# Optimization experiments

Hardware: AMD Instinct MI355X
Metric: run time of the kernel (lower is better)

Reference implementation:

```python
import jax, jax.numpy as jnp
import numpy as np

N, E, G = 10000, 80000, 64
F_IN, D, EA, H = 14, 64, 4, 128


def setup_inputs() -> dict:
    key = jax.random.key(0)
    ks = jax.random.split(key, 16)
    f32 = jnp.float32
    def nrm(k, shape, s=0.1):
        return jax.random.normal(k, shape, f32) * s
    return {
        "x": jax.random.normal(ks[0], (N, F_IN), f32),
        "edge_index": jax.random.randint(ks[1], (2, E), 0, N),
        "edge_attr": jax.random.uniform(ks[2], (E, EA), f32),
        "batch": jnp.sort(jax.random.randint(ks[3], (N,), 0, G)),
        "do_dropout": 0,
        "lin0_w": nrm(ks[4], (F_IN, D)), "lin0_b": jnp.zeros((D,), f32),
        "h1_w": nrm(ks[5], (EA, H)), "h1_b": jnp.zeros((H,), f32),
        "h2_w": nrm(ks[6], (H, D * D), 0.02), "h2_b": jnp.zeros((D * D,), f32),
        "conv_root": nrm(ks[7], (D, D)), "conv_bias": jnp.zeros((D,), f32),
        "gru_w_ih": nrm(ks[8], (3 * D, D)), "gru_w_hh": nrm(ks[9], (3 * D, D)),
        "gru_b_ih": jnp.zeros((3 * D,), f32), "gru_b_hh": jnp.zeros((3 * D,), f32),
        "lstm_w_ih": nrm(ks[10], (4 * D, 2 * D)), "lstm_w_hh": nrm(ks[11], (4 * D, D)),
        "lstm_b_ih": jnp.zeros((4 * D,), f32), "lstm_b_hh": jnp.zeros((4 * D,), f32),
        "lin1_w": nrm(ks[12], (2 * D, D)), "lin1_b": jnp.zeros((D,), f32),
        "lin2_w": nrm(ks[13], (D, 1)), "lin2_b": jnp.zeros((1,), f32),
    }


def _seg_softmax(e, seg, n):
    m = jax.ops.segment_max(e, seg, num_segments=n)
    ex = jnp.exp(e - m[seg])
    s = jax.ops.segment_sum(ex, seg, num_segments=n)
    return ex / s[seg]


def _forward(x, edge_index, edge_attr, batch,
             lin0_w, lin0_b, h1_w, h1_b, h2_w, h2_b, conv_root, conv_bias,
             gru_w_ih, gru_w_hh, gru_b_ih, gru_b_hh,
             lstm_w_ih, lstm_w_hh, lstm_b_ih, lstm_b_hh,
             lin1_w, lin1_b, lin2_w, lin2_b):
    src, tgt = edge_index[0], edge_index[1]
    out = jax.nn.relu(x @ lin0_w + lin0_b)              # [N, D]
    h = out
    # edge-conditioned weights: MLP(edge_attr) -> [E, D, D]
    W_e = (jax.nn.relu(edge_attr @ h1_w + h1_b) @ h2_w + h2_b).reshape(E, D, D)
    deg = jax.ops.segment_sum(jnp.ones((E,), out.dtype), tgt, num_segments=N)
    deg = jnp.maximum(deg, 1.0)[:, None]
    for _ in range(3):
        msg = jnp.einsum("ei,eio->eo", out[src], W_e)   # per-edge matmul
        agg = jax.ops.segment_sum(msg, tgt, num_segments=N) / deg  # mean aggr
        m = jax.nn.relu(agg + out @ conv_root + conv_bias)
        # single GRU step (torch nn.GRU, 1 layer, seq_len=1)
        gi = m @ gru_w_ih.T + gru_b_ih
        gh = h @ gru_w_hh.T + gru_b_hh
        ir, iz, in_ = jnp.split(gi, 3, axis=-1)
        hr, hz, hn = jnp.split(gh, 3, axis=-1)
        r = jax.nn.sigmoid(ir + hr)
        z = jax.nn.sigmoid(iz + hz)
        n = jnp.tanh(in_ + r * hn)
        h = (1.0 - z) * n + z * h
        out = h
    # Set2Set pooling, 3 processing steps
    q_star = jnp.zeros((G, 2 * D), out.dtype)
    hs = jnp.zeros((G, D), out.dtype)
    cs = jnp.zeros((G, D), out.dtype)
    for _ in range(3):
        gates = q_star @ lstm_w_ih.T + lstm_b_ih + hs @ lstm_w_hh.T + lstm_b_hh
        i, f, g, o = jnp.split(gates, 4, axis=-1)
        cs = jax.nn.sigmoid(f) * cs + jax.nn.sigmoid(i) * jnp.tanh(g)
        hs = jax.nn.sigmoid(o) * jnp.tanh(cs)
        q = hs                                          # [G, D]
        e = jnp.sum(out * q[batch], axis=-1)            # [N]
        a = _seg_softmax(e, batch, G)
        r = jax.ops.segment_sum(a[:, None] * out, batch, num_segments=G)
        q_star = jnp.concatenate([q, r], axis=-1)
    y = jax.nn.relu(q_star @ lin1_w + lin1_b)
    # do_dropout=False in this reference (eval mode): dropout is identity
    y = y @ lin2_w + lin2_b
    return y.reshape(-1)


def reference(x, edge_index, edge_attr, batch, do_dropout,
              lin0_w, lin0_b, h1_w, h1_b, h2_w, h2_b, conv_root, conv_bias,
              gru_w_ih, gru_w_hh, gru_b_ih, gru_b_hh,
              lstm_w_ih, lstm_w_hh, lstm_b_ih, lstm_b_hh,
              lin1_w, lin1_b, lin2_w, lin2_b):
    return _forward(x, edge_index, edge_attr, batch,
                    lin0_w, lin0_b, h1_w, h1_b, h2_w, h2_b, conv_root, conv_bias,
                    gru_w_ih, gru_w_hh, gru_b_ih, gru_b_hh,
                    lstm_w_ih, lstm_w_hh, lstm_b_ih, lstm_b_hh,
                    lin1_w, lin1_b, lin2_w, lin2_b)
```

## Files before the change

kernel.cpp:

```cpp
#include <hip/hip_runtime.h>
#include <math.h>

#define N_NODES 10000
#define N_EDGES 80000
#define N_GRAPH 64
#define DD 64
#define HIDW 128
#define F_IN 14
#define EAD 4
#define KSMAX 8

typedef _Float16 f16x8 __attribute__((ext_vector_type(8)));
typedef float f32x4 __attribute__((ext_vector_type(4)));

__device__ __forceinline__ float sigmoidf_(float x){ return 1.0f/(1.0f+expf(-x)); }


__global__ void k_prep_bpack(const float* __restrict__ h2w, _Float16* __restrict__ Bp){
  int idx = blockIdx.x*256 + threadIdx.x;
  if (idx >= (HIDW*DD/32)*4*64*8) return;
  int j = idx & 7, l = (idx >> 3) & 63, cg = (idx >> 9) & 3, st = idx >> 11;
  int k = st*32 + ((l >> 4) << 3) + j;
  int o = cg*16 + (l & 15);
  int h = k >> 6, i = k & 63;
  Bp[idx] = (_Float16)h2w[(size_t)h*4096 + i*64 + o];
}

__global__ void k_prep_wT(const float* __restrict__ gih, const float* __restrict__ ghh,
                          const float* __restrict__ lih, const float* __restrict__ lhh,
                          float* __restrict__ WihT, float* __restrict__ WhhT,
                          float* __restrict__ IhT,  float* __restrict__ HhT){
  int idx = blockIdx.x*256 + threadIdx.x;
  if (idx < 12288){ int k=idx/192, j=idx%192; WihT[idx]=gih[j*64+k]; return; }
  idx -= 12288;
  if (idx < 12288){ int k=idx/192, j=idx%192; WhhT[idx]=ghh[j*64+k]; return; }
  idx -= 12288;
  if (idx < 32768){ int k=idx>>8, j=idx&255; IhT[idx]=lih[j*128+k]; return; }
  idx -= 32768;
  if (idx < 16384){ int k=idx>>8, j=idx&255; HhT[idx]=lhh[j*64+k]; return; }
}


__global__ void k_count(const int* __restrict__ tgt, int* __restrict__ cnt){
  int e = blockIdx.x*256 + threadIdx.x;
  if (e < N_EDGES) atomicAdd(&cnt[tgt[e]], 1);
}

__global__ __launch_bounds__(1024) void k_scan(const int* __restrict__ cnt, int* __restrict__ offs,
                                               int* __restrict__ cursor, float* __restrict__ deg){
  __shared__ int sc[1024];
  int t = threadIdx.x;
  int base = t*10;
  int loc[10]; int tot = 0;
  #pragma unroll
  for (int j=0;j<10;++j){
    int i = base+j;
    int c = (i < N_NODES) ? cnt[i] : 0;
    loc[j] = tot; tot += c;
  }
  sc[t] = tot; __syncthreads();
  for (int st=1; st<1024; st<<=1){
    int v = (t>=st) ? sc[t-st] : 0;
    __syncthreads();
    sc[t] += v;
    __syncthreads();
  }
  int ex = sc[t] - tot;
  #pragma unroll
  for (int j=0;j<10;++j){
    int i = base+j;
    if (i < N_NODES){
      int o = ex + loc[j];
      offs[i] = o; cursor[i] = o;
      int c = cnt[i];
      deg[i] = (float)(c > 0 ? c : 1);
    }
  }
  if (t == 1023) offs[N_NODES] = sc[1023];
}

__global__ void k_sortE(const int* __restrict__ tgt, int* __restrict__ cursor, int* __restrict__ sorted){
  int e = blockIdx.x*256 + threadIdx.x;
  if (e < N_EDGES){ int p = atomicAdd(&cursor[tgt[e]], 1); sorted[p] = e; }
}

__global__ void k_graphoff(const int* __restrict__ batch, int* __restrict__ goff){
  int g = threadIdx.x;
  if (g > N_GRAPH) return;
  int lo = 0, hi = N_NODES;
  while (lo < hi){ int mid = (lo+hi)>>1; if (batch[mid] < g) lo = mid+1; else hi = mid; }
  goff[g] = lo;
}


__global__ __launch_bounds__(256) void k_lin0(const float* __restrict__ x, const float* __restrict__ w,
                                              const float* __restrict__ b, float* __restrict__ s){
  int tid = threadIdx.x;
  int g = tid >> 6, o = tid & 63;
  int n = blockIdx.x*4 + g;
  __shared__ float xL[4][F_IN];
  if (tid < 4*F_IN){
    int gg = tid / F_IN, k = tid % F_IN;
    int nn = blockIdx.x*4 + gg;
    xL[gg][k] = (nn < N_NODES) ? x[nn*F_IN + k] : 0.f;
  }
  __syncthreads();
  if (n >= N_NODES) return;
  float acc = b[o];
  #pragma unroll
  for (int k=0;k<F_IN;++k) acc += xL[g][k]*w[k*64+o];
  s[n*64+o] = fmaxf(acc, 0.f);
}


template<int CH, bool WRITE_S>
__global__ __launch_bounds__(256) void k_aggpre_t(
    const float* __restrict__ s, const float* __restrict__ ea,
    const float* __restrict__ h1_w, const float* __restrict__ h1_b,
    const int* __restrict__ offs, const int* __restrict__ sorted,
    const int* __restrict__ srcA, int c0,
    _Float16* __restrict__ P, float* __restrict__ Ssum){
  constexpr int RH = CH/4;
  int t = blockIdx.x;
  int tid = threadIdx.x;
  int i = tid & 63, hb = tid >> 6;
  __shared__ float sL[4][64];
  __shared__ float hidL[4][CH];
  __shared__ int eIdx[4], sIdx[4];
  float acc[RH];
  #pragma unroll
  for (int r=0;r<RH;++r) acc[r]=0.f;
  float sacc = 0.f;
  int e0 = offs[t], e1 = offs[t+1];
  for (int base = e0; base < e1; base += 4){
    int ecnt = min(4, e1 - base);
    __syncthreads();
    if (tid < ecnt){
      int e = sorted[base + tid];
      eIdx[tid] = e;
      sIdx[tid] = srcA[e];
    }
    __syncthreads();
    if (hb < ecnt) sL[hb][i] = s[(size_t)sIdx[hb]*64 + i];
    for (int a = tid; a < 4*CH; a += 256){
      int j = a / CH, hh = a % CH;
      if (j < ecnt){
        int e = eIdx[j];
        int h = c0 + hh;
        float v = h1_b[h];
        #pragma unroll
        for (int k=0;k<EAD;++k) v += ea[e*EAD+k]*h1_w[k*HIDW + h];
        hidL[j][hh] = fmaxf(v, 0.f);
      }
    }
    __syncthreads();
    for (int j=0;j<ecnt;++j){
      float sv = sL[j][i];
      #pragma unroll
      for (int r=0;r<RH;++r) acc[r] += hidL[j][hb*RH + r]*sv;
      if (WRITE_S && hb==0) sacc += sv;
    }
  }
  _Float16* row = P + (size_t)t*(CH*64);
  #pragma unroll
  for (int r=0;r<RH;++r) row[(hb*RH + r)*64 + i] = (_Float16)acc[r];
  if (WRITE_S && hb==0) Ssum[(size_t)t*64 + i] = sacc;
}

__global__ __launch_bounds__(256) void k_gemm_lds(const _Float16* __restrict__ A,
    const _Float16* __restrict__ Bp, float* __restrict__ Cpart, int K, int first){
  __shared__ _Float16 tile[16*1024];
  int tid = threadIdx.x;
  int y = blockIdx.y;
  const size_t rowBytes = (size_t)K*2;
  {
    int sub = tid >> 7;
    int colb = (tid & 127) * 16;
    const char* Abase = (const char*)A + (size_t)(blockIdx.x*16)*rowBytes + (size_t)y*2048;
    #pragma unroll
    for (int i = 0; i < 8; ++i){
      int r = i*2 + sub;
      f16x8 v = *(const f16x8*)(Abase + (size_t)r*rowBytes + (size_t)(colb ^ ((r&7)<<4)));
      *(f16x8*)((char*)tile + r*2048 + colb) = v;
    }
  }
  __syncthreads();
  int cg = tid >> 6, lane = tid & 63;
  int row = lane & 15, kb = lane >> 4;
  const char* tbase = (const char*)tile + row*2048;
  int swz = (row & 7) << 4;
  f32x4 acc = 0.f;
  int fr0 = y*32*4;
  #pragma unroll 8
  for (int st = 0; st < 32; ++st){
    f16x8 af = *(const f16x8*)(tbase + ((st*64 + kb*16) ^ swz));
    f16x8 bf = *(const f16x8*)(Bp + ((size_t)(fr0 + st*4 + cg)*64 + lane)*8);
    acc = __builtin_amdgcn_mfma_f32_16x16x32_f16(af, bf, acc, 0, 0, 0);
  }
  int crow0 = blockIdx.x*16 + kb*4;
  int ccol = cg*16 + (lane & 15);
  float* base = Cpart + (size_t)y*(N_NODES*64);
  #pragma unroll
  for (int r=0;r<4;++r){
    float* cp = base + (size_t)(crow0 + r)*64 + ccol;
    if (first) *cp = acc[r];
    else       *cp += acc[r];
  }
}

__global__ __launch_bounds__(256) void k_node_update(const float* __restrict__ Cpart,
    const float* __restrict__ Ssum, const float* __restrict__ h2b,
    const float* __restrict__ deg, float* __restrict__ s,
    const float* __restrict__ conv_root, const float* __restrict__ conv_bias,
    const float* __restrict__ WihT, const float* __restrict__ WhhT,
    const float* __restrict__ bih, const float* __restrict__ bhh, int nslots){
  int tid = threadIdx.x;
  int g = tid >> 6, o = tid & 63;
  int n = blockIdx.x*4 + g;
  __shared__ float hS[4][DD];
  __shared__ float mS[4][DD];
  __shared__ float ssS[4][DD];
  bool valid = n < N_NODES;
  float hold = valid ? s[(size_t)n*DD + o] : 0.f;
  hS[g][o] = hold;
  ssS[g][o] = valid ? Ssum[(size_t)n*DD + o] : 0.f;
  __syncthreads();
  float a = 0.f;
  if (valid){
    for (int ks=0; ks<nslots; ++ks) a += Cpart[(size_t)ks*(N_NODES*64) + (size_t)n*64 + o];
  }
  #pragma unroll 8
  for (int k=0;k<DD;++k) a += ssS[g][k]*h2b[k*64+o];
  float dinv = valid ? 1.0f/deg[n] : 0.f;
  float acc = a*dinv + conv_bias[o];
  #pragma unroll 8
  for (int k=0;k<DD;++k) acc += hS[g][k]*conv_root[k*64+o];
  float m = fmaxf(acc, 0.f);
  mS[g][o] = m;
  __syncthreads();
  float gi0 = bih[o], gi1 = bih[64+o], gi2 = bih[128+o];
  float gh0 = bhh[o], gh1 = bhh[64+o], gh2 = bhh[128+o];
  for (int k=0;k<DD;++k){
    float mk = mS[g][k], hk = hS[g][k];
    gi0 += mk*WihT[k*192 + o];      gh0 += hk*WhhT[k*192 + o];
    gi1 += mk*WihT[k*192 + 64 + o]; gh1 += hk*WhhT[k*192 + 64 + o];
    gi2 += mk*WihT[k*192 + 128+ o]; gh2 += hk*WhhT[k*192 + 128+ o];
  }
  float r = sigmoidf_(gi0+gh0);
  float z = sigmoidf_(gi1+gh1);
  float nn = tanhf(gi2 + r*gh2);
  float hnew = (1.f - z)*nn + z*hold;
  if (valid) s[(size_t)n*DD + o] = hnew;
}


__global__ __launch_bounds__(256) void k_set2set(const float* __restrict__ sND,
    const int* __restrict__ goff,
    const float* __restrict__ IhT, const float* __restrict__ HhT,
    const float* __restrict__ bih, const float* __restrict__ bhh,
    float* __restrict__ qstarOut){
  int g = blockIdx.x;
  int tid = threadIdx.x;
  int lane = tid & 63, w = tid >> 6;
  __shared__ float qL[2*DD];
  __shared__ float hL[DD];
  __shared__ float cL[DD];
  __shared__ float gate[256];
  __shared__ float red[4];
  __shared__ float red2[4][DD];
  if (tid < 2*DD) qL[tid] = 0.f;
  if (tid < DD){ hL[tid] = 0.f; cL[tid] = 0.f; }
  __syncthreads();
  int n0 = goff[g], n1 = goff[g+1];
  for (int st = 0; st < 3; ++st){
    float acc = bih[tid] + bhh[tid];
    #pragma unroll 8
    for (int k=0;k<2*DD;++k) acc += qL[k]*IhT[k*256 + tid];
    #pragma unroll 8
    for (int k=0;k<DD;++k)   acc += hL[k]*HhT[k*256 + tid];
    gate[tid] = acc;
    __syncthreads();
    if (tid < DD){
      float i = sigmoidf_(gate[tid]);
      float f = sigmoidf_(gate[64+tid]);
      float gg = tanhf(gate[128+tid]);
      float o = sigmoidf_(gate[192+tid]);
      float c = f*cL[tid] + i*gg;
      float h = o*tanhf(c);
      cL[tid] = c; hL[tid] = h;
    }
    __syncthreads();
    float wmax = -INFINITY;
    for (int n = n0 + w; n < n1; n += 4){
      float p = sND[(size_t)n*DD + lane] * hL[lane];
      #pragma unroll
      for (int s2=32; s2>0; s2>>=1) p += __shfl_xor(p, s2, 64);
      wmax = fmaxf(wmax, p);
    }
    if (lane == 0) red[w] = wmax;
    __syncthreads();
    float m = fmaxf(fmaxf(red[0], red[1]), fmaxf(red[2], red[3]));
    __syncthreads();
    float wsum = 0.f, racc = 0.f;
    for (int n = n0 + w; n < n1; n += 4){
      float outv = sND[(size_t)n*DD + lane];
      float p = outv * hL[lane];
      #pragma unroll
      for (int s2=32; s2>0; s2>>=1) p += __shfl_xor(p, s2, 64);
      float ex = expf(p - m);
      wsum += ex;
      racc += ex * outv;
    }
    if (lane == 0) red[w] = wsum;
    red2[w][lane] = racc;
    __syncthreads();
    if (tid < DD){
      float stot = red[0]+red[1]+red[2]+red[3];
      float rsum = red2[0][tid]+red2[1][tid]+red2[2][tid]+red2[3][tid];
      float r = (stot > 0.f) ? rsum/stot : 0.f;
      qL[tid] = hL[tid];
      qL[DD + tid] = r;
    }
    __syncthreads();
  }
  if (tid < 2*DD) qstarOut[g*2*DD + tid] = qL[tid];
}

__global__ __launch_bounds__(256) void k_final(const float* __restrict__ qstar,
    const float* __restrict__ lin1_w, const float* __restrict__ lin1_b,
    const float* __restrict__ lin2_w, const float* __restrict__ lin2_b,
    float* __restrict__ out){
  __shared__ float red[256];
  int tid = threadIdx.x;
  int g = tid >> 2, part = tid & 3;
  float acc = 0.f;
  for (int d = part*16; d < part*16+16; ++d){
    float z = lin1_b[d];
    #pragma unroll 8
    for (int k=0;k<2*DD;++k) z += qstar[g*2*DD+k]*lin1_w[k*64+d];
    z = fmaxf(z, 0.f);
    acc += z * lin2_w[d];
  }
  red[tid] = acc;
  __syncthreads();
  if (part == 0) out[g] = red[tid]+red[tid+1]+red[tid+2]+red[tid+3] + lin2_b[0];
}


static inline size_t alignup(size_t x){ return (x + 255) & ~(size_t)255; }

extern "C" void kernel_launch(void* const* d_in, const int* in_sizes, int n_in,
                              void* d_out, int out_size, void* d_ws, size_t ws_size,
                              hipStream_t stream){
  const float* x      = (const float*)d_in[0];
  const int*   ei     = (const int*)  d_in[1];
  const float* ea     = (const float*)d_in[2];
  const int*   batch  = (const int*)  d_in[3];
  const float* lin0_w = (const float*)d_in[5];
  const float* lin0_b = (const float*)d_in[6];
  const float* h1_w   = (const float*)d_in[7];
  const float* h1_b   = (const float*)d_in[8];
  const float* h2_w   = (const float*)d_in[9];
  const float* h2_b   = (const float*)d_in[10];
  const float* conv_root = (const float*)d_in[11];
  const float* conv_bias = (const float*)d_in[12];
  const float* gru_w_ih  = (const float*)d_in[13];
  const float* gru_w_hh  = (const float*)d_in[14];
  const float* gru_b_ih  = (const float*)d_in[15];
  const float* gru_b_hh  = (const float*)d_in[16];
  const float* lstm_w_ih = (const float*)d_in[17];
  const float* lstm_w_hh = (const float*)d_in[18];
  const float* lstm_b_ih = (const float*)d_in[19];
  const float* lstm_b_hh = (const float*)d_in[20];
  const float* lin1_w = (const float*)d_in[21];
  const float* lin1_b = (const float*)d_in[22];
  const float* lin2_w = (const float*)d_in[23];
  const float* lin2_b = (const float*)d_in[24];
  (void)in_sizes; (void)n_in; (void)out_size;

  const int* srcA = ei;
  const int* tgtA = ei + N_EDGES;

  char* p = (char*)d_ws;
  size_t off = 0;
  auto take = [&](size_t bytes)->char*{ char* q = p + off; off = alignup(off + bytes); return q; };
  _Float16* Bpack = (_Float16*)take((size_t)(HIDW*DD/32)*4*64*8*2);
  float* sbuf    = (float*)take((size_t)N_NODES*DD*4);
  float* Cpart   = (float*)take((size_t)KSMAX*N_NODES*DD*4);
  float* Ssum    = (float*)take((size_t)N_NODES*DD*4);
  float* WihT    = (float*)take(12288*4);
  float* WhhT    = (float*)take(12288*4);
  float* IhT     = (float*)take(32768*4);
  float* HhT     = (float*)take(16384*4);
  float* deg     = (float*)take(N_NODES*4);
  int*   cnt     = (int*)  take(N_NODES*4);
  int*   offs    = (int*)  take((N_NODES+1)*4);
  int*   cursor  = (int*)  take(N_NODES*4);
  int*   sorted  = (int*)  take(N_EDGES*4);
  int*   goff    = (int*)  take(65*4);
  float* qstar   = (float*)take((size_t)N_GRAPH*2*DD*4);
  size_t fixed_bytes = off;

  int CH = 16;
  const int cands[4] = {128, 64, 32, 16};
  for (int ci = 0; ci < 4; ++ci){
    size_t need = fixed_bytes + (size_t)N_NODES * cands[ci] * 64 * 2;
    if (need <= ws_size){ CH = cands[ci]; break; }
  }
  _Float16* Pbuf = (_Float16*)take((size_t)N_NODES*CH*64*2);
  const int K = CH*64;
  const int nslots = K / 1024;

  hipMemsetAsync(cnt, 0, N_NODES*4, stream);

  k_prep_bpack<<<(HIDW*DD/32)*4*64*8/256, 256, 0, stream>>>(h2_w, Bpack);
  k_prep_wT<<<(12288*2+32768+16384)/256, 256, 0, stream>>>(gru_w_ih, gru_w_hh, lstm_w_ih, lstm_w_hh,
                                                           WihT, WhhT, IhT, HhT);
  k_count<<<(N_EDGES+255)/256, 256, 0, stream>>>(tgtA, cnt);
  k_scan<<<1, 1024, 0, stream>>>(cnt, offs, cursor, deg);
  k_sortE<<<(N_EDGES+255)/256, 256, 0, stream>>>(tgtA, cursor, sorted);
  k_graphoff<<<1, 128, 0, stream>>>(batch, goff);
  k_lin0<<<N_NODES/4, 256, 0, stream>>>(x, lin0_w, lin0_b, sbuf);

  auto launch_agg = [&](int c0, bool writeS){
    dim3 g(N_NODES);
    if (writeS){
      switch (CH){
        case 128: k_aggpre_t<128,true><<<g,256,0,stream>>>(sbuf,ea,h1_w,h1_b,offs,sorted,srcA,c0,Pbuf,Ssum); break;
        case  64: k_aggpre_t< 64,true><<<g,256,0,stream>>>(sbuf,ea,h1_w,h1_b,offs,sorted,srcA,c0,Pbuf,Ssum); break;
        case  32: k_aggpre_t< 32,true><<<g,256,0,stream>>>(sbuf,ea,h1_w,h1_b,offs,sorted,srcA,c0,Pbuf,Ssum); break;
        default : k_aggpre_t< 16,true><<<g,256,0,stream>>>(sbuf,ea,h1_w,h1_b,offs,sorted,srcA,c0,Pbuf,Ssum); break;
      }
    } else {
      switch (CH){
        case 128: k_aggpre_t<128,false><<<g,256,0,stream>>>(sbuf,ea,h1_w,h1_b,offs,sorted,srcA,c0,Pbuf,Ssum); break;
        case  64: k_aggpre_t< 64,false><<<g,256,0,stream>>>(sbuf,ea,h1_w,h1_b,offs,sorted,srcA,c0,Pbuf,Ssum); break;
        case  32: k_aggpre_t< 32,false><<<g,256,0,stream>>>(sbuf,ea,h1_w,h1_b,offs,sorted,srcA,c0,Pbuf,Ssum); break;
        default : k_aggpre_t< 16,false><<<g,256,0,stream>>>(sbuf,ea,h1_w,h1_b,offs,sorted,srcA,c0,Pbuf,Ssum); break;
      }
    }
  };

  for (int it = 0; it < 3; ++it){
    int nch = HIDW / CH;
    for (int c = 0; c < nch; ++c){
      int c0 = c*CH;
      launch_agg(c0, c == 0);
      k_gemm_lds<<<dim3(N_NODES/16, nslots), 256, 0, stream>>>(Pbuf, Bpack + (size_t)(c0*2)*(4*64*8),
                                                               Cpart, K, c == 0);
    }
    k_node_update<<<N_NODES/4, 256, 0, stream>>>(Cpart, Ssum, h2_b, deg, sbuf, conv_root, conv_bias,
                                                 WihT, WhhT, gru_b_ih, gru_b_hh, nslots);
  }

  k_set2set<<<N_GRAPH, 256, 0, stream>>>(sbuf, goff, IhT, HhT, lstm_b_ih, lstm_b_hh, qstar);
  k_final<<<1, 256, 0, stream>>>(qstar, lin1_w, lin1_b, lin2_w, lin2_b, (float*)d_out);
}
```

Before: 743.2 us.

## Precompute edge MLP hidden once, split GEMM partial slots, parallelize set2set

The per-edge hidden layer relu(edge_attr@h1_w+h1_b) is now computed once by a new kernel. It is stored as fp16 in target-sorted order, together with a sorted source index array. This replaces recomputing it inside every aggregation chunk of every message-passing iteration, and the aggregation kernel now processes 8 edges per batch. The GEMM writes each chunk into its own partial slot instead of doing a read-modify-write accumulate. Set2Set is split from one serial per-graph kernel into LSTM, score, exp-sum and readout kernels that spread the node work across the device using atomics. This adds launches and a large fp16 edge buffer, and slightly lowers the precision of the hidden features.

```diff
diff --git a/kernel.cpp b/kernel.cpp
--- a/kernel.cpp
+++ b/kernel.cpp
@@ -14,6 +14,15 @@
 typedef float f32x4 __attribute__((ext_vector_type(4)));
 
 __device__ __forceinline__ float sigmoidf_(float x){ return 1.0f/(1.0f+expf(-x)); }
+
+__device__ __forceinline__ unsigned fkey(float f){
+  unsigned u = __float_as_uint(f);
+  return u ^ ((((int)u) >> 31) | 0x80000000u);
+}
+__device__ __forceinline__ float funkey(unsigned k){
+  unsigned u = (k & 0x80000000u) ? (k ^ 0x80000000u) : ~k;
+  return __uint_as_float(u);
+}
 
 
 __global__ void k_prep_bpack(const float* __restrict__ h2w, _Float16* __restrict__ Bp){
@@ -79,9 +88,14 @@
   if (t == 1023) offs[N_NODES] = sc[1023];
 }
 
-__global__ void k_sortE(const int* __restrict__ tgt, int* __restrict__ cursor, int* __restrict__ sorted){
+__global__ void k_sortE(const int* __restrict__ tgt, const int* __restrict__ src,
+                        int* __restrict__ cursor, int* __restrict__ srcS, int* __restrict__ pos){
   int e = blockIdx.x*256 + threadIdx.x;
-  if (e < N_EDGES){ int p = atomicAdd(&cursor[tgt[e]], 1); sorted[p] = e; }
+  if (e < N_EDGES){
+    int p = atomicAdd(&cursor[tgt[e]], 1);
+    srcS[p] = src[e];
+    pos[e] = p;
+  }
 }
 
 __global__ void k_graphoff(const int* __restrict__ batch, int* __restrict__ goff){
@@ -112,46 +126,51 @@
   s[n*64+o] = fmaxf(acc, 0.f);
 }
 
+__global__ __launch_bounds__(256) void k_hid(const float* __restrict__ ea,
+    const float* __restrict__ h1_w, const float* __restrict__ h1_b,
+    const int* __restrict__ pos, _Float16* __restrict__ hidS){
+  int tid = threadIdx.x;
+  int g = tid >> 7, j = tid & 127;
+  int e = blockIdx.x*2 + g;
+  __shared__ float eL[2][EAD];
+  __shared__ int pL[2];
+  if (tid < 8){ int gg = tid>>2, k = tid&3; eL[gg][k] = ea[(blockIdx.x*2+gg)*EAD + k]; }
+  if (tid < 2) pL[tid] = pos[blockIdx.x*2 + tid];
+  __syncthreads();
+  (void)e;
+  float v = h1_b[j];
+  #pragma unroll
+  for (int k=0;k<EAD;++k) v += eL[g][k]*h1_w[k*HIDW + j];
+  hidS[(size_t)pL[g]*HIDW + j] = (_Float16)fmaxf(v, 0.f);
+}
+
 
 template<int CH, bool WRITE_S>
 __global__ __launch_bounds__(256) void k_aggpre_t(
-    const float* __restrict__ s, const float* __restrict__ ea,
-    const float* __restrict__ h1_w, const float* __restrict__ h1_b,
-    const int* __restrict__ offs, const int* __restrict__ sorted,
-    const int* __restrict__ srcA, int c0,
+    const float* __restrict__ s, const _Float16* __restrict__ hidS,
+    const int* __restrict__ offs, const int* __restrict__ srcS, int c0,
     _Float16* __restrict__ P, float* __restrict__ Ssum){
   constexpr int RH = CH/4;
   int t = blockIdx.x;
   int tid = threadIdx.x;
   int i = tid & 63, hb = tid >> 6;
-  __shared__ float sL[4][64];
-  __shared__ float hidL[4][CH];
-  __shared__ int eIdx[4], sIdx[4];
+  __shared__ float sL[8][64];
+  __shared__ float hidL[8][CH];
   float acc[RH];
   #pragma unroll
   for (int r=0;r<RH;++r) acc[r]=0.f;
   float sacc = 0.f;
   int e0 = offs[t], e1 = offs[t+1];
-  for (int base = e0; base < e1; base += 4){
-    int ecnt = min(4, e1 - base);
+  for (int base = e0; base < e1; base += 8){
+    int ecnt = min(8, e1 - base);
     __syncthreads();
-    if (tid < ecnt){
-      int e = sorted[base + tid];
-      eIdx[tid] = e;
-      sIdx[tid] = srcA[e];
-    }
-    __syncthreads();
-    if (hb < ecnt) sL[hb][i] = s[(size_t)sIdx[hb]*64 + i];
-    for (int a = tid; a < 4*CH; a += 256){
+    for (int a = tid; a < ecnt*64; a += 256){
+      int j = a >> 6, ii = a & 63;
+      sL[j][ii] = s[(size_t)srcS[base+j]*64 + ii];
+    }
+    for (int a = tid; a < ecnt*CH; a += 256){
       int j = a / CH, hh = a % CH;
-      if (j < ecnt){
-        int e = eIdx[j];
-        int h = c0 + hh;
-        float v = h1_b[h];
-        #pragma unroll
-        for (int k=0;k<EAD;++k) v += ea[e*EAD+k]*h1_w[k*HIDW + h];
-        hidL[j][hh] = fmaxf(v, 0.f);
-      }
+      hidL[j][hh] = (float)hidS[(size_t)(base+j)*HIDW + c0 + hh];
     }
     __syncthreads();
     for (int j=0;j<ecnt;++j){
@@ -168,7 +187,7 @@
 }
 
 __global__ __launch_bounds__(256) void k_gemm_lds(const _Float16* __restrict__ A,
-    const _Float16* __restrict__ Bp, float* __restrict__ Cpart, int K, int first){
+    const _Float16* __restrict__ Bp, float* __restrict__ Cpart, int K){
   __shared__ _Float16 tile[16*1024];
   int tid = threadIdx.x;
   int y = blockIdx.y;
@@ -201,11 +220,8 @@
   int ccol = cg*16 + (lane & 15);
   float* base = Cpart + (size_t)y*(N_NODES*64);
   #pragma unroll
-  for (int r=0;r<4;++r){
-    float* cp = base + (size_t)(crow0 + r)*64 + ccol;
-    if (first) *cp = acc[r];
-    else       *cp += acc[r];
-  }
+  for (int r=0;r<4;++r)
+    base[(size_t)(crow0 + r)*64 + ccol] = acc[r];
 }
 
 __global__ __launch_bounds__(256) void k_node_update(const float* __restrict__ Cpart,
@@ -213,7 +229,7 @@
     const float* __restrict__ deg, float* __restrict__ s,
     const float* __restrict__ conv_root, const float* __restrict__ conv_bias,
     const float* __restrict__ WihT, const float* __restrict__ WhhT,
-    const float* __restrict__ bih, const float* __restrict__ bhh, int nslots){
+    const float* __restrict__ bih, const float* __restrict__ bhh){
   int tid = threadIdx.x;
   int g = tid >> 6, o = tid & 63;
   int n = blockIdx.x*4 + g;
@@ -227,7 +243,8 @@
   __syncthreads();
   float a = 0.f;
   if (valid){
-    for (int ks=0; ks<nslots; ++ks) a += Cpart[(size_t)ks*(N_NODES*64) + (size_t)n*64 + o];
+    #pragma unroll
+    for (int ks=0; ks<KSMAX; ++ks) a += Cpart[(size_t)ks*(N_NODES*64) + (size_t)n*64 + o];
   }
   #pragma unroll 8
   for (int k=0;k<DD;++k) a += ssS[g][k]*h2b[k*64+o];
@@ -254,76 +271,105 @@
 }
 
 
-__global__ __launch_bounds__(256) void k_set2set(const float* __restrict__ sND,
-    const int* __restrict__ goff,
+__global__ __launch_bounds__(256) void k_s2s_lstm(const float* __restrict__ qstar,
+    float* __restrict__ hs, float* __restrict__ cs,
     const float* __restrict__ IhT, const float* __restrict__ HhT,
     const float* __restrict__ bih, const float* __restrict__ bhh,
-    float* __restrict__ qstarOut){
+    unsigned* __restrict__ mkey, float* __restrict__ sumb, int first){
   int g = blockIdx.x;
   int tid = threadIdx.x;
-  int lane = tid & 63, w = tid >> 6;
   __shared__ float qL[2*DD];
   __shared__ float hL[DD];
-  __shared__ float cL[DD];
   __shared__ float gate[256];
-  __shared__ float red[4];
+  if (first){
+    if (tid < 2*DD) qL[tid] = 0.f;
+    if (tid < DD)   hL[tid] = 0.f;
+  } else {
+    if (tid < 2*DD) qL[tid] = qstar[g*2*DD + tid];
+    if (tid < DD)   hL[tid] = hs[g*DD + tid];
+  }
+  __syncthreads();
+  float acc = bih[tid] + bhh[tid];
+  #pragma unroll 8
+  for (int k=0;k<2*DD;++k) acc += qL[k]*IhT[k*256 + tid];
+  #pragma unroll 8
+  for (int k=0;k<DD;++k)   acc += hL[k]*HhT[k*256 + tid];
+  gate[tid] = acc;
+  __syncthreads();
+  if (tid < DD){
+    float i = sigmoidf_(gate[tid]);
+    float f = sigmoidf_(gate[64+tid]);
+    float gg = tanhf(gate[128+tid]);
+    float o = sigmoidf_(gate[192+tid]);
+    float cprev = first ? 0.f : cs[g*DD+tid];
+    float c = f*cprev + i*gg;
+    float h = o*tanhf(c);
+    cs[g*DD+tid] = c;
+    hs[g*DD+tid] = h;
+  }
+  if (tid == 64) mkey[g] = fkey(-3.0e38f);
+  if (tid == 65) sumb[g] = 0.f;
+}
+
+__global__ __launch_bounds__(256) void k_s2s_e(const float* __restrict__ sND,
+    const float* __restrict__ hs, const int* __restrict__ batch,
+    float* __restrict__ ebuf, unsigned* __restrict__ mkey){
+  int w = threadIdx.x >> 6, lane = threadIdx.x & 63;
+  int n = blockIdx.x*4 + w;
+  int g = batch[n];
+  float p = sND[(size_t)n*DD + lane] * hs[g*DD + lane];
+  #pragma unroll
+  for (int s2=32; s2>0; s2>>=1) p += __shfl_xor(p, s2, 64);
+  if (lane == 0){
+    ebuf[n] = p;
+    atomicMax(&mkey[g], fkey(p));
+  }
+}
+
+__global__ __launch_bounds__(256) void k_s2s_x(float* __restrict__ ebuf,
+    const int* __restrict__ batch, const unsigned* __restrict__ mkey,
+    float* __restrict__ sumb){
+  int n = blockIdx.x*256 + threadIdx.x;
+  int lane = threadIdx.x & 63;
+  float ex = 0.f; int g = -1;
+  if (n < N_NODES){
+    g = batch[n];
+    float m = funkey(mkey[g]);
+    ex = expf(ebuf[n] - m);
+    ebuf[n] = ex;
+  }
+  int g0 = __shfl(g, 0, 64);
+  bool uni = __all(g == g0);
+  if (uni && g0 >= 0){
+    float t = ex;
+    #pragma unroll
+    for (int s2=32; s2>0; s2>>=1) t += __shfl_xor(t, s2, 64);
+    if (lane == 0) atomicAdd(&sumb[g0], t);
+  } else if (n < N_NODES){
+    atomicAdd(&sumb[g], ex);
+  }
+}
+
+__global__ __launch_bounds__(256) void k_s2s_r(const float* __restrict__ sND,
+    const float* __restrict__ ebuf, const int* __restrict__ goff,
+    const float* __restrict__ hs, const float* __restrict__ sumb,
+    float* __restrict__ qstar){
+  int g = blockIdx.x;
+  int tid = threadIdx.x;
+  int d = tid & 63, w = tid >> 6;
   __shared__ float red2[4][DD];
-  if (tid < 2*DD) qL[tid] = 0.f;
-  if (tid < DD){ hL[tid] = 0.f; cL[tid] = 0.f; }
-  __syncthreads();
   int n0 = goff[g], n1 = goff[g+1];
-  for (int st = 0; st < 3; ++st){
-    float acc = bih[tid] + bhh[tid];
-    #pragma unroll 8
-    for (int k=0;k<2*DD;++k) acc += qL[k]*IhT[k*256 + tid];
-    #pragma unroll 8
-    for (int k=0;k<DD;++k)   acc += hL[k]*HhT[k*256 + tid];
-    gate[tid] = acc;
-    __syncthreads();
-    if (tid < DD){
-      float i = sigmoidf_(gate[tid]);
-      float f = sigmoidf_(gate[64+tid]);
-      float gg = tanhf(gate[128+tid]);
-      float o = sigmoidf_(gate[192+tid]);
-      float c = f*cL[tid] + i*gg;
-      float h = o*tanhf(c);
-      cL[tid] = c; hL[tid] = h;
-    }
-    __syncthreads();
-    float wmax = -INFINITY;
-    for (int n = n0 + w; n < n1; n += 4){
-      float p = sND[(size_t)n*DD + lane] * hL[lane];
-      #pragma unroll
-      for (int s2=32; s2>0; s2>>=1) p += __shfl_xor(p, s2, 64);
-      wmax = fmaxf(wmax, p);
-    }
-    if (lane == 0) red[w] = wmax;
-    __syncthreads();
-    float m = fmaxf(fmaxf(red[0], red[1]), fmaxf(red[2], red[3]));
-    __syncthreads();
-    float wsum = 0.f, racc = 0.f;
-    for (int n = n0 + w; n < n1; n += 4){
-      float outv = sND[(size_t)n*DD + lane];
-      float p = outv * hL[lane];
-      #pragma unroll
-      for (int s2=32; s2>0; s2>>=1) p += __shfl_xor(p, s2, 64);
-      float ex = expf(p - m);
-      wsum += ex;
-      racc += ex * outv;
-    }
-    if (lane == 0) red[w] = wsum;
-    red2[w][lane] = racc;
-    __syncthreads();
-    if (tid < DD){
-      float stot = red[0]+red[1]+red[2]+red[3];
-      float rsum = red2[0][tid]+red2[1][tid]+red2[2][tid]+red2[3][tid];
-      float r = (stot > 0.f) ? rsum/stot : 0.f;
-      qL[tid] = hL[tid];
-      qL[DD + tid] = r;
-    }
-    __syncthreads();
-  }
-  if (tid < 2*DD) qstarOut[g*2*DD + tid] = qL[tid];
+  float racc = 0.f;
+  for (int n = n0 + w; n < n1; n += 4)
+    racc += ebuf[n] * sND[(size_t)n*DD + d];
+  red2[w][d] = racc;
+  __syncthreads();
+  if (tid < DD){
+    float rs = red2[0][d]+red2[1][d]+red2[2][d]+red2[3][d];
+    float st = sumb[g];
+    qstar[g*2*DD + d]      = hs[g*DD + d];
+    qstar[g*2*DD + DD + d] = (st > 0.f) ? rs/st : 0.f;
+  }
 }
 
 __global__ __launch_bounds__(256) void k_final(const float* __restrict__ qstar,
@@ -385,9 +431,10 @@
   size_t off = 0;
   auto take = [&](size_t bytes)->char*{ char* q = p + off; off = alignup(off + bytes); return q; };
   _Float16* Bpack = (_Float16*)take((size_t)(HIDW*DD/32)*4*64*8*2);
-  float* sbuf    = (float*)take((size_t)N_NODES*DD*4);
-  float* Cpart   = (float*)take((size_t)KSMAX*N_NODES*DD*4);
-  float* Ssum    = (float*)take((size_t)N_NODES*DD*4);
+  float* sbuf     = (float*)take((size_t)N_NODES*DD*4);
+  float* Cpart    = (float*)take((size_t)KSMAX*N_NODES*DD*4);
+  float* Ssum     = (float*)take((size_t)N_NODES*DD*4);
+  _Float16* hidS  = (_Float16*)take((size_t)N_EDGES*HIDW*2);
   float* WihT    = (float*)take(12288*4);
   float* WhhT    = (float*)take(12288*4);
   float* IhT     = (float*)take(32768*4);
@@ -396,9 +443,15 @@
   int*   cnt     = (int*)  take(N_NODES*4);
   int*   offs    = (int*)  take((N_NODES+1)*4);
   int*   cursor  = (int*)  take(N_NODES*4);
-  int*   sorted  = (int*)  take(N_EDGES*4);
+  int*   srcS    = (int*)  take(N_EDGES*4);
+  int*   pos     = (int*)  take(N_EDGES*4);
   int*   goff    = (int*)  take(65*4);
   float* qstar   = (float*)take((size_t)N_GRAPH*2*DD*4);
+  float* hsb     = (float*)take((size_t)N_GRAPH*DD*4);
+  float* csb     = (float*)take((size_t)N_GRAPH*DD*4);
+  unsigned* mkey = (unsigned*)take(N_GRAPH*4);
+  float* sumb    = (float*)take(N_GRAPH*4);
+  float* ebuf    = (float*)take(N_NODES*4);
   size_t fixed_bytes = off;
 
   int CH = 16;
@@ -418,25 +471,26 @@
                                                            WihT, WhhT, IhT, HhT);
   k_count<<<(N_EDGES+255)/256, 256, 0, stream>>>(tgtA, cnt);
   k_scan<<<1, 1024, 0, stream>>>(cnt, offs, cursor, deg);
-  k_sortE<<<(N_EDGES+255)/256, 256, 0, stream>>>(tgtA, cursor, sorted);
+  k_sortE<<<(N_EDGES+255)/256, 256, 0, stream>>>(tgtA, srcA, cursor, srcS, pos);
   k_graphoff<<<1, 128, 0, stream>>>(batch, goff);
   k_lin0<<<N_NODES/4, 256, 0, stream>>>(x, lin0_w, lin0_b, sbuf);
+  k_hid<<<N_EDGES/2, 256, 0, stream>>>(ea, h1_w, h1_b, pos, hidS);
 
   auto launch_agg = [&](int c0, bool writeS){
     dim3 g(N_NODES);
     if (writeS){
       switch (CH){
-        case 128: k_aggpre_t<128,true><<<g,256,0,stream>>>(sbuf,ea,h1_w,h1_b,offs,sorted,srcA,c0,Pbuf,Ssum); break;
-        case  64: k_aggpre_t< 64,true><<<g,256,0,stream>>>(sbuf,ea,h1_w,h1_b,offs,sorted,srcA,c0,Pbuf,Ssum); break;
-        case  32: k_aggpre_t< 32,true><<<g,256,0,stream>>>(sbuf,ea,h1_w,h1_b,offs,sorted,srcA,c0,Pbuf,Ssum); break;
-        default : k_aggpre_t< 16,true><<<g,256,0,stream>>>(sbuf,ea,h1_w,h1_b,offs,sorted,srcA,c0,Pbuf,Ssum); break;
+        case 128: k_aggpre_t<128,true><<<g,256,0,stream>>>(sbuf,hidS,offs,srcS,c0,Pbuf,Ssum); break;
+        case  64: k_aggpre_t< 64,true><<<g,256,0,stream>>>(sbuf,hidS,offs,srcS,c0,Pbuf,Ssum); break;
+        case  32: k_aggpre_t< 32,true><<<g,256,0,stream>>>(sbuf,hidS,offs,srcS,c0,Pbuf,Ssum); break;
+        default : k_aggpre_t< 16,true><<<g,256,0,stream>>>(sbuf,hidS,offs,srcS,c0,Pbuf,Ssum); break;
       }
     } else {
       switch (CH){
-        case 128: k_aggpre_t<128,false><<<g,256,0,stream>>>(sbuf,ea,h1_w,h1_b,offs,sorted,srcA,c0,Pbuf,Ssum); break;
-        case  64: k_aggpre_t< 64,false><<<g,256,0,stream>>>(sbuf,ea,h1_w,h1_b,offs,sorted,srcA,c0,Pbuf,Ssum); break;
-        case  32: k_aggpre_t< 32,false><<<g,256,0,stream>>>(sbuf,ea,h1_w,h1_b,offs,sorted,srcA,c0,Pbuf,Ssum); break;
-        default : k_aggpre_t< 16,false><<<g,256,0,stream>>>(sbuf,ea,h1_w,h1_b,offs,sorted,srcA,c0,Pbuf,Ssum); break;
+        case 128: k_aggpre_t<128,false><<<g,256,0,stream>>>(sbuf,hidS,offs,srcS,c0,Pbuf,Ssum); break;
+        case  64: k_aggpre_t< 64,false><<<g,256,0,stream>>>(sbuf,hidS,offs,srcS,c0,Pbuf,Ssum); break;
+        case  32: k_aggpre_t< 32,false><<<g,256,0,stream>>>(sbuf,hidS,offs,srcS,c0,Pbuf,Ssum); break;
+        default : k_aggpre_t< 16,false><<<g,256,0,stream>>>(sbuf,hidS,offs,srcS,c0,Pbuf,Ssum); break;
       }
     }
   };
@@ -446,13 +500,20 @@
     for (int c = 0; c < nch; ++c){
       int c0 = c*CH;
       launch_agg(c0, c == 0);
-      k_gemm_lds<<<dim3(N_NODES/16, nslots), 256, 0, stream>>>(Pbuf, Bpack + (size_t)(c0*2)*(4*64*8),
-                                                               Cpart, K, c == 0);
+      k_gemm_lds<<<dim3(N_NODES/16, nslots), 256, 0, stream>>>(
+          Pbuf, Bpack + (size_t)(c0*2)*(4*64*8),
+          Cpart + (size_t)(c*nslots)*(N_NODES*64), K);
     }
     k_node_update<<<N_NODES/4, 256, 0, stream>>>(Cpart, Ssum, h2_b, deg, sbuf, conv_root, conv_bias,
-                                                 WihT, WhhT, gru_b_ih, gru_b_hh, nslots);
-  }
-
-  k_set2set<<<N_GRAPH, 256, 0, stream>>>(sbuf, goff, IhT, HhT, lstm_b_ih, lstm_b_hh, qstar);
+                                                 WihT, WhhT, gru_b_ih, gru_b_hh);
+  }
+
+  for (int st = 0; st < 3; ++st){
+    k_s2s_lstm<<<N_GRAPH, 256, 0, stream>>>(qstar, hsb, csb, IhT, HhT, lstm_b_ih, lstm_b_hh,
+                                            mkey, sumb, st == 0);
+    k_s2s_e<<<N_NODES/4, 256, 0, stream>>>(sbuf, hsb, batch, ebuf, mkey);
+    k_s2s_x<<<(N_NODES+255)/256, 256, 0, stream>>>(ebuf, batch, mkey, sumb);
+    k_s2s_r<<<N_GRAPH, 256, 0, stream>>>(sbuf, ebuf, goff, hsb, sumb, qstar);
+  }
   k_final<<<1, 256, 0, stream>>>(qstar, lin1_w, lin1_b, lin2_w, lin2_b, (float*)d_out);
 }
```

After: 981.5 us. +32.1%, slower.
